# Optimization experiments

Measured on AMD Instinct MI355X. Metric: run time of the kernel, lower is better.

Reference implementation:

```python
import jax, jax.numpy as jnp
import numpy as np

H = W = 512
A = 256  # number of projection angles


def setup_inputs() -> dict:
    key = jax.random.key(0)
    k1, k2 = jax.random.split(key)
    data = jax.random.normal(k1, (1, 1, H, W), dtype=jnp.float32)
    # angles uniform in [0, pi) -- realistic tomographic scan range
    angles = jax.random.uniform(k2, (A,), dtype=jnp.float32) * np.float32(np.pi)
    return {"data": data, "angles": angles}


def _radon(data, angles):
    B, C, h, w = data.shape  # B == C == 1 structurally required by the torch module
    nA = angles.shape[0]
    cos = jnp.cos(angles)
    sin = jnp.sin(angles)

    # F.affine_grid(align_corners=False) base coordinates: pixel centers in [-1, 1]
    xs = (2.0 * jnp.arange(w, dtype=data.dtype) + 1.0) / w - 1.0  # [W]
    ys = (2.0 * jnp.arange(h, dtype=data.dtype) + 1.0) / h - 1.0  # [H]
    by, bx = jnp.meshgrid(ys, xs, indexing="ij")  # [H,W]

    # theta built from -angles: rows [cos a, sin a, 0; -sin a, cos a, 0]
    gx = cos[:, None, None] * bx + sin[:, None, None] * by  # [A,H,W]
    gy = -sin[:, None, None] * bx + cos[:, None, None] * by  # [A,H,W]

    # grid_sample(align_corners=False): unnormalize to input pixel coords
    ix = ((gx + 1.0) * w - 1.0) * 0.5
    iy = ((gy + 1.0) * h - 1.0) * 0.5

    x0 = jnp.floor(ix).astype(jnp.int32)
    y0 = jnp.floor(iy).astype(jnp.int32)
    x1 = x0 + 1
    y1 = y0 + 1
    wx1 = ix - x0.astype(data.dtype)
    wx0 = 1.0 - wx1
    wy1 = iy - y0.astype(data.dtype)
    wy0 = 1.0 - wy1

    img = data[0, 0]  # [H,W]

    def gather(yy, xx):
        # zero padding: out-of-range taps contribute 0
        valid = (xx >= 0) & (xx < w) & (yy >= 0) & (yy < h)
        v = img[jnp.clip(yy, 0, h - 1), jnp.clip(xx, 0, w - 1)]
        return jnp.where(valid, v, jnp.zeros((), data.dtype))

    rotated = (wy0 * (wx0 * gather(y0, x0) + wx1 * gather(y0, x1))
               + wy1 * (wx0 * gather(y1, x0) + wx1 * gather(y1, x1)))  # [A,H,W]

    proj = jnp.sum(rotated, axis=1)  # sum over height -> [A,W]
    return proj.reshape(1, 1, nA, w)


def reference(data, angles):
    return _radon(data, angles)
```

## Files before the change

kernel.cpp:

```cpp
#include <hip/hip_runtime.h>


#define HH 512
#define WW 512
#define NA 256
#define XC 64
#define YC 64
#define NXC (WW / XC)
#define NYC (HH / YC)
#define NW 8
#define ROWS_MAX 92
#define STRIDE_MAX 97
#define PAD 112
#define PW (WW + 2 * PAD)
#define PH (HH + 2 * PAD)

typedef float f32x2 __attribute__((ext_vector_type(2)));

__global__ __launch_bounds__(256) void pad_kernel(
    const float* __restrict__ img, float* __restrict__ P)
{
    const int c = blockIdx.x * 256 + threadIdx.x;
    const int r = blockIdx.y;
    if (c >= PW) return;
    const int gr = r - PAD, gc = c - PAD;
    float v = 0.0f;
    if ((unsigned)gr < (unsigned)HH && (unsigned)gc < (unsigned)WW)
        v = img[gr * WW + gc];
    P[r * PW + c] = v;
}

__device__ __forceinline__ float fract_f(float x) {
#if __has_builtin(__builtin_amdgcn_fractf)
    return __builtin_amdgcn_fractf(x);
#else
    return x - floorf(x);
#endif
}

template <bool PADDED, int STRIDE>
__device__ __forceinline__ void radon_body(
    const float* __restrict__ src, float* __restrict__ tile,
    const float s, const float c, const int lane, const int wid, const int x0,
    float& acc0, float& acc1)
{
    const float u  = (float)(x0 + lane) + (0.5f - 256.0f);
    const float u0 = (float)x0 + (0.5f - 256.0f);
    const float u1 = u0 + (float)(XC - 1);

    const float* __restrict__ Porg = PADDED ? (src + PAD * PW + PAD) : src;

    for (int yc = 0; yc < NYC; ++yc) {
        const float v0 = (float)(yc * YC) + (0.5f - 256.0f);
        const float v1 = v0 + (float)(YC - 1);

        const float cu0 = c * u0, cu1 = c * u1;
        const float sv0 = s * v0, sv1 = s * v1;
        const float su0 = -s * u0, su1 = -s * u1;
        const float cv0 = c * v0, cv1 = c * v1;

        const float cx_min = fminf(cu0, cu1) + fminf(sv0, sv1) + 255.5f;
        const float cx_max = fmaxf(cu0, cu1) + fmaxf(sv0, sv1) + 255.5f;
        const float rx_min = fminf(su0, su1) + fminf(cv0, cv1) + 255.5f;
        const float rx_max = fmaxf(su0, su1) + fmaxf(cv0, cv1) + 255.5f;

        const int c_lo = (int)floorf(cx_min);
        const int c_hi = (int)floorf(cx_max) + 1;
        const int r_lo = (int)floorf(rx_min);
        const int r_hi = (int)floorf(rx_max) + 1;
        int bh = min(r_hi - r_lo + 1, ROWS_MAX);

        if (c_lo > WW - 1 || c_hi < 0 || r_lo > HH - 1 || r_hi < 0) continue;

        __syncthreads();

        if (PADDED) {
            if (lane < 23) {
                for (int r = wid; r < bh; r += NW) {
                    const float* g = Porg + (r_lo + r) * PW + c_lo + lane * 4;
                    float* l = &tile[r * STRIDE];
                    __builtin_amdgcn_global_load_lds(
                        (__attribute__((address_space(1))) const void*)g,
                        (__attribute__((address_space(3))) void*)l, 16, 0, 0);
                }
            }
        } else {
            const int bw = min(c_hi - c_lo + 1, STRIDE_MAX);
            for (int r = wid; r < bh; r += NW) {
                const int gr = r_lo + r;
                const bool row_ok = ((unsigned)gr < (unsigned)HH);
                const float* __restrict__ rowp = src + gr * WW;
                for (int cc = lane; cc < bw; cc += 64) {
                    const int gc = c_lo + cc;
                    float v = 0.0f;
                    if (row_ok) {
                        const int gcl = min(max(gc, 0), WW - 1);
                        const float t = rowp[gcl];
                        v = ((unsigned)gc < (unsigned)WW) ? t : 0.0f;
                    }
                    tile[r * STRIDE + cc] = v;
                }
            }
        }

        __syncthreads();

        const float bc = fmaf(c, u, 255.5f - (float)c_lo);
        const float br = fmaf(-s, u, 255.5f - (float)r_lo);
        const float vy0 = v0 + (float)(wid * 8);

        f32x2 crx;
        crx.x = fmaf(s, vy0, bc);
        crx.y = fmaf(c, vy0, br);
        f32x2 step;
        step.x = s;
        step.y = c;

#pragma unroll
        for (int i = 0; i < 8; ++i) {
            const float cxl = crx.x;
            const float rxl = crx.y;
            const int ci = (int)cxl;
            const int ri = (int)rxl;
            const float wx1 = fract_f(cxl);
            const float wy1 = fract_f(rxl);

            __builtin_assume(ri >= 0 && ri < ROWS_MAX);
            __builtin_assume(ci >= 0 && ci < STRIDE_MAX);
            const int ad = ri * STRIDE + ci;

            f32x2 top, bot;
            top.x = tile[ad];
            top.y = tile[ad + 1];
            bot.x = tile[ad + STRIDE];
            bot.y = tile[ad + STRIDE + 1];

            f32x2 wyv;
            wyv.x = wy1;
            wyv.y = wy1;
            const f32x2 pv = __builtin_elementwise_fma(wyv, bot - top, top);

            acc0 += pv.x;
            acc1 = fmaf(wx1, pv.y - pv.x, acc1);

            crx += step;
        }
    }
}

template <bool PADDED>
__global__ __launch_bounds__(512, 8) void radon_kernel(
    const float* __restrict__ src,
    const float* __restrict__ angles, float* __restrict__ out)
{
    __shared__ float tile[ROWS_MAX * STRIDE_MAX];

    const int tid  = threadIdx.x;
    const int lane = tid & 63;
    const int wid  = tid >> 6;

    const int a  = blockIdx.x >> 3;
    const int x0 = (blockIdx.x & 7) * XC;

    float s, c;
    sincosf(angles[a], &s, &c);

    float acc0 = 0.0f, acc1 = 0.0f;
    if (c >= 0.0f)
        radon_body<PADDED, 95>(src, tile, s, c, lane, wid, x0, acc0, acc1);
    else
        radon_body<PADDED, 97>(src, tile, s, c, lane, wid, x0, acc0, acc1);

    __syncthreads();
    tile[tid] = acc0 + acc1;
    __syncthreads();
    if (tid < 64) {
        float r = tile[tid];
#pragma unroll
        for (int k = 1; k < NW; ++k) r += tile[k * 64 + tid];
        out[a * WW + x0 + tid] = r;
    }
}

extern "C" void kernel_launch(void* const* d_in, const int* in_sizes, int n_in,
                              void* d_out, int out_size, void* d_ws, size_t ws_size,
                              hipStream_t stream) {
    const float* img    = (const float*)d_in[0];
    const float* angles = (const float*)d_in[1];
    float* out = (float*)d_out;
    float* P   = (float*)d_ws;

    const bool padded = (ws_size >= (size_t)PW * PH * sizeof(float));

    if (padded) {
        pad_kernel<<<dim3((PW + 255) / 256, PH), 256, 0, stream>>>(img, P);
        radon_kernel<true><<<dim3(NA * NXC), 512, 0, stream>>>(P, angles, out);
    } else {
        radon_kernel<false><<<dim3(NA * NXC), 512, 0, stream>>>(img, angles, out);
    }
}
```

Measured before the change: 109.5 us.

## Double-buffer LDS tiles with smaller y-chunks to overlap staging and sampling

Splits each angle strip into 11 row chunks of 48 rows (last chunk 32) and double-buffers the LDS tile. The next chunk's bounding box is staged with async global_load_lds while the current chunk is sampled, which removes one barrier per chunk. Bounding-box math is specialised on the sign of cos, and the per-row staging address is now incremented instead of recomputed. LDS use doubles and launch bounds drop to 4 blocks per CU, so occupancy falls, and the smaller chunks add per-chunk overhead.

```diff
diff --git a/kernel.cpp b/kernel.cpp
--- a/kernel.cpp
+++ b/kernel.cpp
@@ -5,12 +5,13 @@
 #define WW 512
 #define NA 256
 #define XC 64
-#define YC 64
 #define NXC (WW / XC)
-#define NYC (HH / YC)
 #define NW 8
-#define ROWS_MAX 92
-#define STRIDE_MAX 97
+#define YC 48
+#define NCH 11
+#define LASTR 32
+#define ROWS_MAX 82
+#define SMAX 97
 #define PAD 112
 #define PW (WW + 2 * PAD)
 #define PH (HH + 2 * PAD)
@@ -38,122 +39,163 @@
 #endif
 }
 
+struct BB {
+    int c_lo, r_lo, bh, bw;
+    bool valid;
+    float v0;
+};
+
+template <int STRIDE, int NYS>
+__device__ __forceinline__ void sample_chunk(
+    const float* __restrict__ tb, const BB& b,
+    const float s, const float c, const float u, const int wid,
+    float& acc0, float& acc1)
+{
+    const float bc = fmaf(c, u, 255.5f - (float)b.c_lo);
+    const float br = fmaf(-s, u, 255.5f - (float)b.r_lo);
+    const float vy0 = b.v0 + (float)(wid * NYS);
+
+    f32x2 crx, stepv;
+    crx.x = fmaf(s, vy0, bc);
+    crx.y = fmaf(c, vy0, br);
+    stepv.x = s;
+    stepv.y = c;
+
+#pragma unroll
+    for (int i = 0; i < NYS; ++i) {
+        const float cxl = crx.x;
+        const float rxl = crx.y;
+        const int ci = (int)cxl;
+        const int ri = (int)rxl;
+        const float wx1 = fract_f(cxl);
+        const float wy1 = fract_f(rxl);
+
+        __builtin_assume(ri >= 0 && ri < ROWS_MAX);
+        __builtin_assume(ci >= 0 && ci < SMAX);
+        const int ad = ri * STRIDE + ci;
+
+        f32x2 top, bot;
+        top.x = tb[ad];
+        top.y = tb[ad + 1];
+        bot.x = tb[ad + STRIDE];
+        bot.y = tb[ad + STRIDE + 1];
+
+        f32x2 wyv;
+        wyv.x = wy1;
+        wyv.y = wy1;
+        const f32x2 pv = __builtin_elementwise_fma(wyv, bot - top, top);
+
+        acc0 += pv.x;
+        acc1 = fmaf(wx1, pv.y - pv.x, acc1);
+
+        crx += stepv;
+    }
+}
+
 template <bool PADDED, int STRIDE>
 __device__ __forceinline__ void radon_body(
     const float* __restrict__ src, float* __restrict__ tile,
     const float s, const float c, const int lane, const int wid, const int x0,
     float& acc0, float& acc1)
 {
+    constexpr bool CPOS = (STRIDE == 95);
+
     const float u  = (float)(x0 + lane) + (0.5f - 256.0f);
     const float u0 = (float)x0 + (0.5f - 256.0f);
     const float u1 = u0 + (float)(XC - 1);
 
     const float* __restrict__ Porg = PADDED ? (src + PAD * PW + PAD) : src;
 
-    for (int yc = 0; yc < NYC; ++yc) {
-        const float v0 = (float)(yc * YC) + (0.5f - 256.0f);
-        const float v1 = v0 + (float)(YC - 1);
-
-        const float cu0 = c * u0, cu1 = c * u1;
-        const float sv0 = s * v0, sv1 = s * v1;
-        const float su0 = -s * u0, su1 = -s * u1;
-        const float cv0 = c * v0, cv1 = c * v1;
-
-        const float cx_min = fminf(cu0, cu1) + fminf(sv0, sv1) + 255.5f;
-        const float cx_max = fmaxf(cu0, cu1) + fmaxf(sv0, sv1) + 255.5f;
-        const float rx_min = fminf(su0, su1) + fminf(cv0, cv1) + 255.5f;
-        const float rx_max = fmaxf(su0, su1) + fmaxf(cv0, cv1) + 255.5f;
-
-        const int c_lo = (int)floorf(cx_min);
+    auto bbox = [&](int k) -> BB {
+        BB b;
+        const int rows = (k == NCH - 1) ? LASTR : YC;
+        b.v0 = (float)(k * YC) - 255.5f;
+        const float v1 = b.v0 + (float)(rows - 1);
+        float cx_min, cx_max, rx_min, rx_max;
+        if (CPOS) {
+            cx_min = fmaf(c, u0, fmaf(s, b.v0, 255.5f));
+            cx_max = fmaf(c, u1, fmaf(s, v1,   255.5f));
+            rx_min = fmaf(-s, u1, fmaf(c, b.v0, 255.5f));
+            rx_max = fmaf(-s, u0, fmaf(c, v1,   255.5f));
+        } else {
+            cx_min = fmaf(c, u1, fmaf(s, b.v0, 255.5f));
+            cx_max = fmaf(c, u0, fmaf(s, v1,   255.5f));
+            rx_min = fmaf(-s, u1, fmaf(c, v1,   255.5f));
+            rx_max = fmaf(-s, u0, fmaf(c, b.v0, 255.5f));
+        }
+        b.c_lo = (int)floorf(cx_min);
+        b.r_lo = (int)floorf(rx_min);
         const int c_hi = (int)floorf(cx_max) + 1;
-        const int r_lo = (int)floorf(rx_min);
         const int r_hi = (int)floorf(rx_max) + 1;
-        int bh = min(r_hi - r_lo + 1, ROWS_MAX);
-
-        if (c_lo > WW - 1 || c_hi < 0 || r_lo > HH - 1 || r_hi < 0) continue;
-
-        __syncthreads();
-
+        b.bh = min(r_hi - b.r_lo + 1, ROWS_MAX);
+        b.bw = min(c_hi - b.c_lo + 1, SMAX);
+        b.valid = (b.c_lo <= WW - 1) & (c_hi >= 0) & (b.r_lo <= HH - 1) & (r_hi >= 0);
+        return b;
+    };
+
+    auto stage = [&](int buf, const BB& b) {
+        float* __restrict__ base = tile + buf * (ROWS_MAX * SMAX);
         if (PADDED) {
-            if (lane < 23) {
-                for (int r = wid; r < bh; r += NW) {
-                    const float* g = Porg + (r_lo + r) * PW + c_lo + lane * 4;
-                    float* l = &tile[r * STRIDE];
+            if (lane < 21) {
+                const float* g = Porg + (b.r_lo + wid) * PW + b.c_lo + lane * 4;
+                float* l = base + wid * STRIDE;
+                for (int r = wid; r < b.bh; r += NW) {
                     __builtin_amdgcn_global_load_lds(
                         (__attribute__((address_space(1))) const void*)g,
                         (__attribute__((address_space(3))) void*)l, 16, 0, 0);
+                    g += NW * PW;
+                    l += NW * STRIDE;
                 }
             }
         } else {
-            const int bw = min(c_hi - c_lo + 1, STRIDE_MAX);
-            for (int r = wid; r < bh; r += NW) {
-                const int gr = r_lo + r;
+            for (int r = wid; r < b.bh; r += NW) {
+                const int gr = b.r_lo + r;
                 const bool row_ok = ((unsigned)gr < (unsigned)HH);
                 const float* __restrict__ rowp = src + gr * WW;
-                for (int cc = lane; cc < bw; cc += 64) {
-                    const int gc = c_lo + cc;
+                for (int cc = lane; cc < b.bw; cc += 64) {
+                    const int gc = b.c_lo + cc;
                     float v = 0.0f;
                     if (row_ok) {
                         const int gcl = min(max(gc, 0), WW - 1);
                         const float t = rowp[gcl];
                         v = ((unsigned)gc < (unsigned)WW) ? t : 0.0f;
                     }
-                    tile[r * STRIDE + cc] = v;
+                    base[r * STRIDE + cc] = v;
                 }
             }
         }
+    };
+
+    BB cur = bbox(0);
+    if (cur.valid) stage(0, cur);
+
+#pragma unroll 1
+    for (int k = 0; k < NCH; ++k) {
+        BB nxt;
+        nxt.valid = false;
+        if (k + 1 < NCH) nxt = bbox(k + 1);
 
         __syncthreads();
 
-        const float bc = fmaf(c, u, 255.5f - (float)c_lo);
-        const float br = fmaf(-s, u, 255.5f - (float)r_lo);
-        const float vy0 = v0 + (float)(wid * 8);
-
-        f32x2 crx;
-        crx.x = fmaf(s, vy0, bc);
-        crx.y = fmaf(c, vy0, br);
-        f32x2 step;
-        step.x = s;
-        step.y = c;
-
-#pragma unroll
-        for (int i = 0; i < 8; ++i) {
-            const float cxl = crx.x;
-            const float rxl = crx.y;
-            const int ci = (int)cxl;
-            const int ri = (int)rxl;
-            const float wx1 = fract_f(cxl);
-            const float wy1 = fract_f(rxl);
-
-            __builtin_assume(ri >= 0 && ri < ROWS_MAX);
-            __builtin_assume(ci >= 0 && ci < STRIDE_MAX);
-            const int ad = ri * STRIDE + ci;
-
-            f32x2 top, bot;
-            top.x = tile[ad];
-            top.y = tile[ad + 1];
-            bot.x = tile[ad + STRIDE];
-            bot.y = tile[ad + STRIDE + 1];
-
-            f32x2 wyv;
-            wyv.x = wy1;
-            wyv.y = wy1;
-            const f32x2 pv = __builtin_elementwise_fma(wyv, bot - top, top);
-
-            acc0 += pv.x;
-            acc1 = fmaf(wx1, pv.y - pv.x, acc1);
-
-            crx += step;
+        if (nxt.valid) stage((k + 1) & 1, nxt);
+
+        if (cur.valid) {
+            const float* tb = tile + (k & 1) * (ROWS_MAX * SMAX);
+            if (k == NCH - 1)
+                sample_chunk<STRIDE, LASTR / NW>(tb, cur, s, c, u, wid, acc0, acc1);
+            else
+                sample_chunk<STRIDE, YC / NW>(tb, cur, s, c, u, wid, acc0, acc1);
         }
+        cur = nxt;
     }
 }
 
 template <bool PADDED>
-__global__ __launch_bounds__(512, 8) void radon_kernel(
+__global__ __launch_bounds__(512, 4) void radon_kernel(
     const float* __restrict__ src,
     const float* __restrict__ angles, float* __restrict__ out)
 {
-    __shared__ float tile[ROWS_MAX * STRIDE_MAX];
+    __shared__ float tile[2 * ROWS_MAX * SMAX];
 
     const int tid  = threadIdx.x;
     const int lane = tid & 63;
```

After: 126.1 us. +15.2%, slower.
